# Kernel optimization log

Measured on AMD Instinct MI355X. Metric: run time of the kernel, lower is better.

The kernel has to match this reference:

```python
import jax, jax.numpy as jnp
import numpy as np

DIM = 512
HEADS = 8
DHEAD = 64
WIN = 128
QK_SCALE = 8.0
LN_EPS = 1e-5


def setup_inputs() -> dict:
    key = jax.random.key(0)
    ks = jax.random.split(key, 5)
    B, N = 8, 4096
    x = jax.random.normal(ks[0], (B, N, DIM), jnp.float32)
    w_qkv = jax.random.normal(ks[1], (3 * HEADS * DHEAD, DIM), jnp.float32) * 0.02
    w_out = jax.random.normal(ks[2], (DIM, HEADS * DHEAD), jnp.float32) * 0.02
    b_out = jnp.zeros((DIM,), jnp.float32)
    w_ff1 = jax.random.normal(ks[3], (4 * DIM, DIM), jnp.float32) * 0.02
    w_ff2 = jax.random.normal(ks[4], (DIM, 4 * DIM), jnp.float32) * 0.02
    return {
        'x': x, 'w_qkv': w_qkv,
        'q_scale': jnp.ones((DHEAD,), jnp.float32),
        'k_scale': jnp.ones((DHEAD,), jnp.float32),
        'w_out': w_out, 'b_out': b_out,
        'ln1_g': jnp.ones((DIM,), jnp.float32), 'ln1_b': jnp.zeros((DIM,), jnp.float32),
        'ff_ln_g': jnp.ones((DIM,), jnp.float32), 'ff_ln_b': jnp.zeros((DIM,), jnp.float32),
        'w_ff1': w_ff1, 'w_ff2': w_ff2,
    }


def _ln(x, g, b):
    m = jnp.mean(x, axis=-1, keepdims=True)
    v = jnp.mean((x - m) ** 2, axis=-1, keepdims=True)
    return (x - m) * jax.lax.rsqrt(v + LN_EPS) * g + b


def _l2norm(t):
    return t / jnp.clip(jnp.linalg.norm(t, axis=-1, keepdims=True), 1e-12)


def _rotary(t, pos):
    # t: (B, H, N, DHEAD); standard (non-xpos) rotary, half-split style
    inv_freq = 1.0 / (10000.0 ** (jnp.arange(0, DHEAD, 2, dtype=jnp.float32) / DHEAD))
    freqs = pos[:, None] * inv_freq                      # (N, DHEAD/2)
    emb = jnp.concatenate([freqs, freqs], axis=-1)       # (N, DHEAD)
    cos, sin = jnp.cos(emb), jnp.sin(emb)
    t1, t2 = t[..., : DHEAD // 2], t[..., DHEAD // 2:]
    rot = jnp.concatenate([-t2, t1], axis=-1)
    return t * cos + rot * sin


def reference(x, w_qkv, q_scale, k_scale, w_out, b_out, ln1_g, ln1_b,
              ff_ln_g, ff_ln_b, w_ff1, w_ff2):
    B, N, D = x.shape
    nw = N // WIN

    # ---- LocalMHA (prenorm, qk-rmsnorm, sliding window, causal) ----
    h = _ln(x, ln1_g, ln1_b)
    qkv = h @ w_qkv.T                                    # (B, N, 3*H*DHEAD)
    q, k, v = jnp.split(qkv, 3, axis=-1)

    def to_heads(t):
        return t.reshape(B, N, HEADS, DHEAD).transpose(0, 2, 1, 3)  # (B,H,N,d)

    q, k, v = to_heads(q), to_heads(k), to_heads(v)
    q = _l2norm(q) * q_scale
    k = _l2norm(k) * k_scale
    pos = jnp.arange(N, dtype=jnp.float32)
    q = _rotary(q, pos)
    k = _rotary(k, pos)

    # bucket into windows; keys/values look back one window
    bq = q.reshape(B, HEADS, nw, WIN, DHEAD)
    bk = k.reshape(B, HEADS, nw, WIN, DHEAD)
    bv = v.reshape(B, HEADS, nw, WIN, DHEAD)

    def look_back(t):
        prev = jnp.concatenate([jnp.zeros_like(t[:, :, :1]), t[:, :, :-1]], axis=2)
        return jnp.concatenate([prev, t], axis=3)

    kk, vv = look_back(bk), look_back(bv)

    qpos = jnp.arange(N, dtype=jnp.int32).reshape(nw, WIN)
    kprev = jnp.concatenate([jnp.full((1, WIN), -1, jnp.int32), qpos[:-1]], axis=0)
    kpos = jnp.concatenate([kprev, qpos], axis=1)
    mask = (qpos[:, :, None] >= kpos[:, None, :]) & (kpos[:, None, :] >= 0)

    sim = jnp.einsum('bhnid,bhnjd->bhnij', bq, kk) * QK_SCALE
    sim = jnp.where(mask, sim, -1e9)
    attn = jax.nn.softmax(sim, axis=-1)
    out = jnp.einsum('bhnij,bhnjd->bhnid', attn, vv)
    out = out.reshape(B, HEADS, N, DHEAD).transpose(0, 2, 1, 3).reshape(B, N, HEADS * DHEAD)
    x = x + out @ w_out.T + b_out

    # ---- FeedForward: LN -> Linear(4D, no bias) -> GELU -> Linear(D, no bias) ----
    hf = _ln(x, ff_ln_g, ff_ln_b)
    ff = jax.nn.gelu(hf @ w_ff1.T, approximate=False) @ w_ff2.T
    return x + ff
```

## Files before the change

### kernel.cpp

```cpp
#include <hip/hip_runtime.h>
#include <cstdint>
#include <cstddef>

typedef __bf16 bf16;
typedef __bf16 bf16x8 __attribute__((ext_vector_type(8)));
typedef float f32x4 __attribute__((ext_vector_type(4)));

#define DEV static __device__ __forceinline__

constexpr int BATCH = 8;
constexpr int SEQ = 4096;
constexpr int DIM = 512;
constexpr int HEADS = 8;
constexpr int DH = 64;
constexpr int WIN = 128;
constexpr int NW = SEQ / WIN;
constexpr int TOK = BATCH * SEQ;
constexpr float EPS = 1e-5f;

constexpr size_t R_EL   = (size_t)TOK * DIM;
constexpr size_t C_QKV  = 0;
constexpr size_t C_WOUT = 786432;
constexpr size_t C_WF1  = 1048576;
constexpr size_t C_WF2  = 2097152;
constexpr size_t C_SM   = 3145728;
constexpr size_t P_EL   = 3148416;

DEV void gload_lds16(const void* g, void* l) {
  __builtin_amdgcn_global_load_lds((__attribute__((address_space(1))) void*)g,
                                   (__attribute__((address_space(3))) void*)l,
                                   16, 0, 0);
}

DEV f32x4 mfma16(bf16x8 a, bf16x8 b, f32x4 c) {
  return __builtin_amdgcn_mfma_f32_16x16x32_bf16(a, b, c, 0, 0, 0);
}

DEV float fast_gelu(float v) {
  const float z = fabsf(v) * 0.7071067811865476f;
  const float t = __builtin_amdgcn_rcpf(1.0f + 0.3275911f * z);
  const float p = t * (0.254829592f +
                  t * (-0.284496736f +
                  t * (1.421413741f +
                  t * (-1.453152027f +
                  t * 1.061405429f))));
  const float e = __expf(-z * z);
  const float erfa = 1.0f - p * e;
  const float cdf = 0.5f + copysignf(0.5f * erfa, v);
  return v * cdf;
}

struct SrcPtrs { const void* p[12]; };

DEV void copy8(const void* src, long si, bf16* dst, bool f32) {
  if (f32) {
    const float4* s = (const float4*)((const float*)src + si);
    float4 a = s[0], b = s[1];
    bf16x8 o;
    o[0] = (bf16)a.x; o[1] = (bf16)a.y; o[2] = (bf16)a.z; o[3] = (bf16)a.w;
    o[4] = (bf16)b.x; o[5] = (bf16)b.y; o[6] = (bf16)b.z; o[7] = (bf16)b.w;
    *(bf16x8*)dst = o;
  } else {
    *(bf16x8*)dst = *(const bf16x8*)((const bf16*)src + si);
  }
}

__global__ __launch_bounds__(256) void ingest_kernel(SrcPtrs sp, bf16* cano) {
  const bool f32 = (((const unsigned short*)sp.p[2])[0] == 0);
  const long e = (long)threadIdx.x * 8;
  int b = blockIdx.x;
  if (b < 384)  { long o = (long)b * 2048 + e; copy8(sp.p[1], o, cano + C_QKV + o, f32); return; }
  b -= 384;
  if (b < 128)  { long o = (long)b * 2048 + e; copy8(sp.p[4], o, cano + C_WOUT + o, f32); return; }
  b -= 128;
  if (b < 512)  { long o = (long)b * 2048 + e; copy8(sp.p[10], o, cano + C_WF1 + o, f32); return; }
  b -= 512;
  if (b < 512)  { long o = (long)b * 2048 + e; copy8(sp.p[11], o, cano + C_WF2 + o, f32); return; }
  b -= 512;
  const long o = (long)b * 2048 + e;
  if (o >= 2688) return;
  const void* src; long si;
  if      (o < 64)   { src = sp.p[2]; si = o; }
  else if (o < 128)  { src = sp.p[3]; si = o - 64; }
  else if (o < 640)  { src = sp.p[5]; si = o - 128; }
  else if (o < 1152) { src = sp.p[6]; si = o - 640; }
  else if (o < 1664) { src = sp.p[7]; si = o - 1152; }
  else if (o < 2176) { src = sp.p[8]; si = o - 1664; }
  else               { src = sp.p[9]; si = o - 2176; }
  copy8(src, si, cano + C_SM + o, f32);
}

__global__ __launch_bounds__(256) void ln_kernel(const void* __restrict__ in,
                                                 const bf16* __restrict__ gg,
                                                 const bf16* __restrict__ bb,
                                                 bf16* __restrict__ out,
                                                 const unsigned short* __restrict__ probe,
                                                 int raw) {
  const int wave = threadIdx.x >> 6, lane = threadIdx.x & 63;
  const int row = blockIdx.x * 4 + wave;
  const size_t base = (size_t)row * DIM + lane * 8;
  float f[8];
  if (raw && probe[0] == 0) {
    const float4* p = (const float4*)((const float*)in + base);
    float4 a = p[0], bq = p[1];
    f[0] = a.x; f[1] = a.y; f[2] = a.z; f[3] = a.w;
    f[4] = bq.x; f[5] = bq.y; f[6] = bq.z; f[7] = bq.w;
  } else {
    bf16x8 v = *(const bf16x8*)((const bf16*)in + base);
#pragma unroll
    for (int i = 0; i < 8; ++i) f[i] = (float)v[i];
  }
  float s = 0.f, sq = 0.f;
#pragma unroll
  for (int i = 0; i < 8; ++i) { s += f[i]; sq += f[i] * f[i]; }
#pragma unroll
  for (int m = 32; m; m >>= 1) { s += __shfl_xor(s, m); sq += __shfl_xor(sq, m); }
  const float mean = s * (1.0f / DIM);
  const float var = fmaxf(sq * (1.0f / DIM) - mean * mean, 0.0f);
  const float rs = rsqrtf(var + EPS);
  bf16x8 gv = *(const bf16x8*)(gg + lane * 8);
  bf16x8 bv = *(const bf16x8*)(bb + lane * 8);
  bf16x8 o;
#pragma unroll
  for (int i = 0; i < 8; ++i) o[i] = (bf16)((f[i] - mean) * rs * (float)gv[i] + (float)bv[i]);
  *(bf16x8*)((bf16*)out + base) = o;
}

template <int MODE>
__global__ __launch_bounds__(256) void gemm_bt(const bf16* __restrict__ A,
                                               const bf16* __restrict__ Bw,
                                               bf16* __restrict__ O0, bf16* __restrict__ O1,
                                               bf16* __restrict__ O2,
                                               float* __restrict__ Of,
                                               const void* __restrict__ Xraw,
                                               const bf16* __restrict__ Xb,
                                               const bf16* __restrict__ bias,
                                               const unsigned short* __restrict__ probe,
                                               int K, int bstride, int ostride, int gx) {
  __shared__ __align__(16) bf16 smem[4 * 128 * 32];
  const int tid = threadIdx.x;
  const int wave = tid >> 6, lane = tid & 63;
  const int l15 = lane & 15, quad = lane >> 4;
  const int id = blockIdx.x;
  const int per = gx * 8;
  const int tM = ((id / per) * 8 + (id & 7)) * 128;
  const int tN = ((id % per) >> 3) * 128;
  const int wM = (wave >> 1) * 64, wN = (wave & 1) * 64;
  f32x4 acc[4][4];
  const f32x4 z = {0.f, 0.f, 0.f, 0.f};
#pragma unroll
  for (int i = 0; i < 4; ++i)
#pragma unroll
    for (int j = 0; j < 4; ++j) acc[i][j] = z;

  auto stage = [&](int k0, int p) {
    bf16* dA = smem + p * 8192;
    bf16* dB = dA + 4096;
#pragma unroll
    for (int t = 0; t < 2; ++t) {
      const int c = tid + t * 256;
      const int row = c >> 2, cc = (c & 3) * 8;
      gload_lds16(A + (size_t)(tM + row) * K + k0 + cc, &dA[c * 8]);
      gload_lds16(Bw + (size_t)(tN + row) * bstride + k0 + cc, &dB[c * 8]);
    }
  };

  stage(0, 0);
  int cur = 0;
  for (int k0 = 0; k0 < K; k0 += 32) {
    __syncthreads();
    if (k0 + 32 < K) stage(k0 + 32, cur ^ 1);
    const bf16* As = smem + cur * 8192;
    const bf16* Bs = As + 4096;
    bf16x8 aF[4], bF[4];
#pragma unroll
    for (int i = 0; i < 4; ++i) aF[i] = *(const bf16x8*)&As[(wM + i * 16 + l15) * 32 + quad * 8];
#pragma unroll
    for (int j = 0; j < 4; ++j) bF[j] = *(const bf16x8*)&Bs[(wN + j * 16 + l15) * 32 + quad * 8];
#pragma unroll
    for (int i = 0; i < 4; ++i)
#pragma unroll
      for (int j = 0; j < 4; ++j) acc[i][j] = mfma16(aF[i], bF[j], acc[i][j]);
    cur ^= 1;
  }

  if constexpr (MODE == 0) {
    bf16* ob = smem + wave * 1152;
    const int colbase = tN + wN;
    const int which = colbase >> 9;
    const int head = (colbase >> 6) & 7;
    bf16* dst = which == 0 ? O0 : (which == 1 ? O1 : O2);
    const int ch = lane & 7;
    float scv[8], invf[8];
    if (which < 2) {
      const bf16* sc = which ? bias : Xb;
      bf16x8 s8 = *(const bf16x8*)(sc + ch * 8);
#pragma unroll
      for (int u = 0; u < 8; ++u) {
        scv[u] = (float)s8[u] * (which == 0 ? 8.0f : 1.0f);
        invf[u] = exp2f(-(float)((ch & 3) * 8 + u) * (13.287712379549449f / 32.0f));
      }
    }
#pragma unroll
    for (int i = 0; i < 4; ++i) {
#pragma unroll
      for (int j = 0; j < 4; ++j)
#pragma unroll
        for (int r = 0; r < 4; ++r)
          ob[(quad * 4 + r) * 72 + j * 16 + l15] = (bf16)acc[i][j][r];
#pragma unroll
      for (int t = 0; t < 2; ++t) {
        const int rr = t * 8 + (lane >> 3);
        const int rowg = tM + wM + i * 16 + rr;
        bf16x8 ov = *(const bf16x8*)&ob[rr * 72 + ch * 8];
        float f[8];
#pragma unroll
        for (int u = 0; u < 8; ++u) f[u] = (float)ov[u];
        if (which < 2) {
          float ss = 0.f;
#pragma unroll
          for (int u = 0; u < 8; ++u) ss += f[u] * f[u];
          ss += __shfl_xor(ss, 1); ss += __shfl_xor(ss, 2); ss += __shfl_xor(ss, 4);
          const float rs = 1.0f / fmaxf(sqrtf(ss), 1e-12f);
#pragma unroll
          for (int u = 0; u < 8; ++u) f[u] *= rs * scv[u];
          float pf[8];
#pragma unroll
          for (int u = 0; u < 8; ++u) pf[u] = __shfl_xor(f[u], 4);
          const float pos = (float)(rowg & (SEQ - 1));
#pragma unroll
          for (int u = 0; u < 8; ++u) {
            float sn, cs;
            __sincosf(pos * invf[u], &sn, &cs);
            const float rot = (ch < 4) ? -pf[u] : pf[u];
            f[u] = f[u] * cs + rot * sn;
          }
        }
        bf16x8 o8;
#pragma unroll
        for (int u = 0; u < 8; ++u) o8[u] = (bf16)f[u];
        const int bb = rowg >> 12, n = rowg & (SEQ - 1);
        *(bf16x8*)(dst + ((size_t)(bb * HEADS + head) * SEQ + n) * DH + ch * 8) = o8;
      }
    }
    return;
  }

  if constexpr (MODE == 1 || MODE == 2) {
    bf16* ob = smem + wave * 1152;
    const int ch = lane & 7;
    bf16x8 bias8;
    bool xf32 = false;
    if constexpr (MODE == 1) {
      bias8 = *(const bf16x8*)(bias + tN + wN + ch * 8);
      xf32 = (probe[0] == 0);
    }
#pragma unroll
    for (int i = 0; i < 4; ++i) {
#pragma unroll
      for (int j = 0; j < 4; ++j)
#pragma unroll
        for (int r = 0; r < 4; ++r)
          ob[(quad * 4 + r) * 72 + j * 16 + l15] = (bf16)acc[i][j][r];
#pragma unroll
      for (int t = 0; t < 2; ++t) {
        const int rr = t * 8 + (lane >> 3);
        const int rowg = tM + wM + i * 16 + rr;
        bf16x8 ov = *(const bf16x8*)&ob[rr * 72 + ch * 8];
        bf16x8 o8;
        if constexpr (MODE == 1) {
          const size_t idx = (size_t)rowg * DIM + tN + wN + ch * 8;
          float xr[8];
          if (xf32) {
            const float4* xp = (const float4*)((const float*)Xraw + idx);
            float4 a = xp[0], bq = xp[1];
            xr[0] = a.x; xr[1] = a.y; xr[2] = a.z; xr[3] = a.w;
            xr[4] = bq.x; xr[5] = bq.y; xr[6] = bq.z; xr[7] = bq.w;
          } else {
            bf16x8 xv = *(const bf16x8*)((const bf16*)Xraw + idx);
#pragma unroll
            for (int u = 0; u < 8; ++u) xr[u] = (float)xv[u];
          }
#pragma unroll
          for (int u = 0; u < 8; ++u) o8[u] = (bf16)((float)ov[u] + xr[u] + (float)bias8[u]);
          *(bf16x8*)(O0 + idx) = o8;
        } else {
#pragma unroll
          for (int u = 0; u < 8; ++u) o8[u] = (bf16)fast_gelu((float)ov[u]);
          *(bf16x8*)(O0 + (size_t)rowg * ostride + tN + wN + ch * 8) = o8;
        }
      }
    }
    return;
  }

  if constexpr (MODE == 3 || MODE == 4) {
    float* obf = (float*)smem + wave * 1024;
    const int ch = lane & 7;
#pragma unroll
    for (int i = 0; i < 4; ++i) {
#pragma unroll
      for (int j = 0; j < 4; ++j)
#pragma unroll
        for (int r = 0; r < 4; ++r)
          obf[(quad * 4 + r) * 64 + j * 16 + l15] = acc[i][j][r];
#pragma unroll
      for (int t = 0; t < 2; ++t) {
        const int rr = t * 8 + (lane >> 3);
        const int rowg = tM + wM + i * 16 + rr;
        const size_t idx = (size_t)rowg * DIM + tN + wN + ch * 8;
        const float4* rp = (const float4*)&obf[rr * 64 + ch * 8];
        float4 a = rp[0], b = rp[1];
        float f[8] = {a.x, a.y, a.z, a.w, b.x, b.y, b.z, b.w};
        if constexpr (MODE == 3) {
          bf16x8 xv = *(const bf16x8*)(Xb + idx);
#pragma unroll
          for (int u = 0; u < 8; ++u) f[u] += (float)xv[u];
        } else {
          const float4* op = (const float4*)(Of + idx);
          float4 oa = op[0], ob4 = op[1];
          f[0] += oa.x; f[1] += oa.y; f[2] += oa.z; f[3] += oa.w;
          f[4] += ob4.x; f[5] += ob4.y; f[6] += ob4.z; f[7] += ob4.w;
        }
        float4 o0 = {f[0], f[1], f[2], f[3]}, o1 = {f[4], f[5], f[6], f[7]};
        ((float4*)(Of + idx))[0] = o0;
        ((float4*)(Of + idx))[1] = o1;
      }
    }
    return;
  }
}

__global__ __launch_bounds__(256, 3) void attn_kernel(const bf16* __restrict__ q,
                                                      const bf16* __restrict__ k,
                                                      const bf16* __restrict__ v,
                                                      bf16* __restrict__ ao) {
  __shared__ __align__(16) bf16 kv[256 * 72];
  __shared__ __align__(16) bf16 pbuf[4][16 * 136];
  const int w = blockIdx.x, h = blockIdx.y, b = blockIdx.z;
  const int tid = threadIdx.x;
  const int wv = tid >> 6, lane = tid & 63;
  const int l15 = lane & 15, quad = lane >> 4;
  const size_t bh = (size_t)b * HEADS + h;
  const bf16* qb = q + bh * SEQ * DH;
  const bf16* kb = k + bh * SEQ * DH;
  const bf16* vb = v + bh * SEQ * DH;
  const int t0 = (w - 1) * WIN;

#pragma unroll
  for (int it = 0; it < 8; ++it) {
    const int c = it * 256 + tid;
    const int tok = c >> 3, ch = c & 7;
    int gt = t0 + tok; gt = gt < 0 ? 0 : gt;
    *(bf16x8*)&kv[tok * 72 + ch * 8] = *(const bf16x8*)(kb + (size_t)gt * DH + ch * 8);
  }
  bf16x8 aQ[2][2];
#pragma unroll
  for (int qt = 0; qt < 2; ++qt) {
    const int qtok = w * WIN + wv * 32 + qt * 16 + l15;
#pragma unroll
    for (int ks = 0; ks < 2; ++ks)
      aQ[qt][ks] = *(const bf16x8*)(qb + (size_t)qtok * DH + ks * 32 + quad * 8);
  }
  int gtv = t0 + tid; gtv = gtv < 0 ? 0 : gtv;
  bf16x8 vld[8];
#pragma unroll
  for (int dg = 0; dg < 8; ++dg)
    vld[dg] = *(const bf16x8*)(vb + (size_t)gtv * DH + dg * 8);
  __syncthreads();

  bf16x8 aP[2][8];
#pragma unroll
  for (int qt = 0; qt < 2; ++qt) {
    f32x4 sreg[16];
#pragma unroll
    for (int nt = 0; nt < 16; ++nt) {
      f32x4 a = {0.f, 0.f, 0.f, 0.f};
#pragma unroll
      for (int ks = 0; ks < 2; ++ks) {
        bf16x8 bK = *(const bf16x8*)&kv[(nt * 16 + l15) * 72 + ks * 32 + quad * 8];
        a = mfma16(aQ[qt][ks], bK, a);
      }
      sreg[nt] = a;
    }
    const int qlb = wv * 32 + qt * 16 + quad * 4;
    float rinv[4];
#pragma unroll
    for (int r = 0; r < 4; ++r) {
      const int ql = qlb + r;
      float sum = 0.f;
#pragma unroll
      for (int nt = 0; nt < 16; ++nt) {
        const int j = nt * 16 + l15;
        const bool valid = (nt < 8) ? (w > 0) : (ql >= j - WIN);
        const float p = valid ? __expf(sreg[nt][r]) : 0.0f;
        sreg[nt][r] = p;
        sum += p;
      }
#pragma unroll
      for (int m = 8; m; m >>= 1) sum += __shfl_xor(sum, m);
      rinv[r] = 1.0f / sum;
    }
#pragma unroll
    for (int half = 0; half < 2; ++half) {
#pragma unroll
      for (int ntw = 0; ntw < 8; ++ntw)
#pragma unroll
        for (int r = 0; r < 4; ++r)
          pbuf[wv][(quad * 4 + r) * 136 + ntw * 16 + l15] =
              (bf16)(sreg[half * 8 + ntw][r] * rinv[r]);
#pragma unroll
      for (int kk = 0; kk < 4; ++kk)
        aP[qt][half * 4 + kk] = *(const bf16x8*)&pbuf[wv][l15 * 136 + kk * 32 + quad * 8];
    }
  }
  __syncthreads();

#pragma unroll
  for (int dg = 0; dg < 8; ++dg)
#pragma unroll
    for (int i = 0; i < 8; ++i)
      kv[(dg * 8 + i) * 264 + tid] = vld[dg][i];
  __syncthreads();

#pragma unroll
  for (int qt = 0; qt < 2; ++qt) {
#pragma unroll
    for (int dt = 0; dt < 4; ++dt) {
      f32x4 o = {0.f, 0.f, 0.f, 0.f};
#pragma unroll
      for (int ks2 = 0; ks2 < 8; ++ks2) {
        bf16x8 bV = *(const bf16x8*)&kv[(dt * 16 + l15) * 264 + ks2 * 32 + quad * 8];
        o = mfma16(aP[qt][ks2], bV, o);
      }
#pragma unroll
      for (int r = 0; r < 4; ++r)
        pbuf[wv][(quad * 4 + r) * 136 + dt * 16 + l15] = (bf16)o[r];
    }
#pragma unroll
    for (int t = 0; t < 2; ++t) {
      const int rr = t * 8 + (lane >> 3), ch = lane & 7;
      bf16x8 ov = *(const bf16x8*)&pbuf[wv][rr * 136 + ch * 8];
      const int tok = w * WIN + wv * 32 + qt * 16 + rr;
      *(bf16x8*)(ao + ((size_t)b * SEQ + tok) * DIM + h * DH + ch * 8) = ov;
    }
  }
}

extern "C" void kernel_launch(void* const* d_in, const int* in_sizes, int n_in,
                              void* d_out, int out_size, void* d_ws, size_t ws_size,
                              hipStream_t stream) {
  (void)in_sizes; (void)n_in; (void)out_size;
  float* out = (float*)d_out;
  bf16* cano = (bf16*)d_ws;
  const unsigned short* probe = (const unsigned short*)d_in[2];

  SrcPtrs sp;
  for (int i = 0; i < 12; ++i) sp.p[i] = d_in[i];

  bf16* slot0 = cano + P_EL;
  bf16* slot1 = cano + P_EL + R_EL;
  bf16* slot2 = cano + P_EL + 2 * R_EL;
  bf16* slot3 = cano + P_EL + 3 * R_EL;

  const bf16* qsc  = cano + C_SM + 0;
  const bf16* ksc  = cano + C_SM + 64;
  const bf16* bout = cano + C_SM + 128;
  const bf16* l1g  = cano + C_SM + 640;
  const bf16* l1b  = cano + C_SM + 1152;
  const bf16* lfg  = cano + C_SM + 1664;
  const bf16* lfb  = cano + C_SM + 2176;

  ingest_kernel<<<1538, 256, 0, stream>>>(sp, cano);
  ln_kernel<<<TOK / 4, 256, 0, stream>>>(d_in[0], l1g, l1b, slot0, probe, 1);
  gemm_bt<0><<<12 * 256, 256, 0, stream>>>(slot0, cano + C_QKV, slot1, slot2, slot3,
                                           nullptr, nullptr, qsc, ksc, probe,
                                           DIM, DIM, 0, 12);
  attn_kernel<<<dim3(NW, HEADS, BATCH), 256, 0, stream>>>(slot1, slot2, slot3, slot0);
  gemm_bt<1><<<4 * 256, 256, 0, stream>>>(slot0, cano + C_WOUT, slot1, nullptr, nullptr,
                                          nullptr, d_in[0], nullptr, bout, probe,
                                          DIM, DIM, 0, 4);
  ln_kernel<<<TOK / 4, 256, 0, stream>>>(slot1, lfg, lfb, slot0, probe, 0);

  const bool big = ws_size >= (size_t)(P_EL + 6 * R_EL) * 2;
  if (big) {
    bf16* f1 = slot2;
    gemm_bt<2><<<16 * 256, 256, 0, stream>>>(slot0, cano + C_WF1, f1, nullptr, nullptr,
                                             nullptr, nullptr, nullptr, nullptr, probe,
                                             DIM, DIM, 2048, 16);
    gemm_bt<3><<<4 * 256, 256, 0, stream>>>(f1, cano + C_WF2, nullptr, nullptr, nullptr,
                                            out, nullptr, slot1, nullptr, probe,
                                            2048, 2048, 0, 4);
  } else {
    bf16* f1h = slot2;
    for (int half = 0; half < 2; ++half) {
      const bf16* w1h = cano + C_WF1 + (size_t)half * 1024 * DIM;
      const bf16* w2h = cano + C_WF2 + (size_t)half * 1024;
      gemm_bt<2><<<8 * 256, 256, 0, stream>>>(slot0, w1h, f1h, nullptr, nullptr,
                                              nullptr, nullptr, nullptr, nullptr, probe,
                                              DIM, DIM, 1024, 8);
      if (half == 0)
        gemm_bt<3><<<4 * 256, 256, 0, stream>>>(f1h, w2h, nullptr, nullptr, nullptr,
                                                out, nullptr, slot1, nullptr, probe,
                                                1024, 2048, 0, 4);
      else
        gemm_bt<4><<<4 * 256, 256, 0, stream>>>(f1h, w2h, nullptr, nullptr, nullptr,
                                                out, nullptr, nullptr, nullptr, probe,
                                                1024, 2048, 0, 4);
    }
  }
}
```

Before: 509.9 us.

## Triple-buffer GEMM K-loop with explicit vmcnt waits and single barrier

Moves the bf16 GEMM main loop from double to triple buffering in LDS, prefetching two K-tiles ahead. A raw s_waitcnt vmcnt plus s_barrier, fenced by sched_barrier, replaces __syncthreads, so loads of the next-next tile stay in flight while the current one is consumed. The epilogue scratch is pointed at the free buffer. The cost is more LDS per block (48KB), which may lower occupancy, and the hand-tuned vmcnt counts assume exactly four async loads per stage.

```diff
diff --git a/kernel.cpp b/kernel.cpp
--- a/kernel.cpp
+++ b/kernel.cpp
@@ -137,7 +137,7 @@
                                                const bf16* __restrict__ bias,
                                                const unsigned short* __restrict__ probe,
                                                int K, int bstride, int ostride, int gx) {
-  __shared__ __align__(16) bf16 smem[4 * 128 * 32];
+  __shared__ __align__(16) bf16 smem[3 * 8192];
   const int tid = threadIdx.x;
   const int wave = tid >> 6, lane = tid & 63;
   const int l15 = lane & 15, quad = lane >> 4;
@@ -153,23 +153,33 @@
 #pragma unroll
     for (int j = 0; j < 4; ++j) acc[i][j] = z;
 
-  auto stage = [&](int k0, int p) {
+  auto stage = [&](int t, int p) {
+    const int k0 = t * 32;
     bf16* dA = smem + p * 8192;
     bf16* dB = dA + 4096;
 #pragma unroll
-    for (int t = 0; t < 2; ++t) {
-      const int c = tid + t * 256;
+    for (int tt = 0; tt < 2; ++tt) {
+      const int c = tid + tt * 256;
       const int row = c >> 2, cc = (c & 3) * 8;
       gload_lds16(A + (size_t)(tM + row) * K + k0 + cc, &dA[c * 8]);
       gload_lds16(Bw + (size_t)(tN + row) * bstride + k0 + cc, &dB[c * 8]);
     }
   };
 
+  const int nt = K >> 5;
   stage(0, 0);
+  stage(1, 1);
+  __builtin_amdgcn_sched_barrier(0);
+  asm volatile("s_waitcnt vmcnt(4)" ::: "memory");
+  __builtin_amdgcn_s_barrier();
+  __builtin_amdgcn_sched_barrier(0);
+
   int cur = 0;
-  for (int k0 = 0; k0 < K; k0 += 32) {
-    __syncthreads();
-    if (k0 + 32 < K) stage(k0 + 32, cur ^ 1);
+  for (int t = 0; t < nt; ++t) {
+    if (t + 2 < nt) {
+      int nx = cur + 2; if (nx >= 3) nx -= 3;
+      stage(t + 2, nx);
+    }
     const bf16* As = smem + cur * 8192;
     const bf16* Bs = As + 4096;
     bf16x8 aF[4], bF[4];
@@ -181,11 +191,19 @@
     for (int i = 0; i < 4; ++i)
 #pragma unroll
       for (int j = 0; j < 4; ++j) acc[i][j] = mfma16(aF[i], bF[j], acc[i][j]);
-    cur ^= 1;
-  }
+    if (t < nt - 1) {
+      __builtin_amdgcn_sched_barrier(0);
+      if (t + 2 < nt) asm volatile("s_waitcnt vmcnt(4)" ::: "memory");
+      else            asm volatile("s_waitcnt vmcnt(0)" ::: "memory");
+      __builtin_amdgcn_s_barrier();
+      __builtin_amdgcn_sched_barrier(0);
+    }
+    ++cur; if (cur == 3) cur = 0;
+  }
+  bf16* eb = smem + cur * 8192;
 
   if constexpr (MODE == 0) {
-    bf16* ob = smem + wave * 1152;
+    bf16* ob = eb + wave * 1152;
     const int colbase = tN + wN;
     const int which = colbase >> 9;
     const int head = (colbase >> 6) & 7;
@@ -247,7 +265,7 @@
   }
 
   if constexpr (MODE == 1 || MODE == 2) {
-    bf16* ob = smem + wave * 1152;
+    bf16* ob = eb + wave * 1152;
     const int ch = lane & 7;
     bf16x8 bias8;
     bool xf32 = false;
@@ -295,7 +313,7 @@
   }
 
   if constexpr (MODE == 3 || MODE == 4) {
-    float* obf = (float*)smem + wave * 1024;
+    float* obf = (float*)eb + wave * 1024;
     const int ch = lane & 7;
 #pragma unroll
     for (int i = 0; i < 4; ++i) {
```

New measurement: 505.9 us. No clear change (-0.8%).
